# Kernel tuning notes

Hardware: AMD Instinct MI355X
Metric: run time of the kernel (lower is better)

## Reference

```python
import jax, jax.numpy as jnp
import numpy as np

B, NG, DEG, CW, OUT = 8, 16384, 16, 64, 256  # graphs, nodes/graph, avg degree, conv_width, output_dim


def _sage(x, src, dst, mask, Wl, bl, Wr):
    # PyG SAGEConv: mean-aggregate neighbors (src -> dst), lin_l(agg)+bias + lin_r(x)
    N = x.shape[0]
    s = jax.ops.segment_sum(x[src] * mask[:, None], dst, num_segments=N)
    c = jax.ops.segment_sum(mask, dst, num_segments=N)
    mean = s / jnp.maximum(c, 1.0)[:, None]
    return mean @ Wl.T + bl + x @ Wr.T


def _gcn(x, src, dst, mask, W, b):
    # PyG GCNConv: self-loops + symmetric deg^{-1/2} normalization; edge_weight == mask
    N = x.shape[0]
    xw = x @ W.T
    deg = 1.0 + jax.ops.segment_sum(mask, dst, num_segments=N)
    dis = jax.lax.rsqrt(deg)
    norm = dis[src] * mask * dis[dst]
    out = jax.ops.segment_sum(xw[src] * norm[:, None], dst, num_segments=N)
    return out + xw * (dis * dis)[:, None] + b


def _topk(x, src, dst, mask, w, n):
    # PyG TopKPooling: score = tanh(x.w/||w||), keep top ceil(0.5*n) per graph,
    # gate kept features by score, re-index edges (here: fixed-size edges + mask)
    score = jnp.tanh((x @ w) / jnp.linalg.norm(w))
    k = (n + 1) // 2
    vals, idx = jax.lax.top_k(score.reshape(B, n), k)  # [B,k], descending like PyG
    perm = (idx + (jnp.arange(B) * n)[:, None]).reshape(-1)  # global old indices
    x_new = x[perm] * vals.reshape(-1)[:, None]
    newpos = jnp.full((B * n,), -1, jnp.int32).at[perm].set(
        jnp.arange(B * k, dtype=jnp.int32))
    ns, nd = newpos[src], newpos[dst]
    m = mask * ((ns >= 0) & (nd >= 0)).astype(x.dtype)
    return x_new, jnp.maximum(ns, 0), jnp.maximum(nd, 0), m, k


def _readout(x, k):
    # [global_max_pool, global_mean_pool] per graph
    xr = x.reshape(B, k, -1)
    return jnp.concatenate([xr.max(axis=1), xr.mean(axis=1)], axis=1)


def setup_inputs() -> dict:
    key = jax.random.key(0)
    ks = jax.random.split(key, 24)
    N, Eg = B * NG, NG * DEG
    off = (jnp.arange(B) * NG)[:, None]
    src = (jax.random.randint(ks[0], (B, Eg), 0, NG) + off).reshape(-1)
    dst = (jax.random.randint(ks[1], (B, Eg), 0, NG) + off).reshape(-1)
    edge_index = jnp.stack([src, dst]).astype(jnp.int32)
    x = jax.random.normal(ks[2], (N, 2), jnp.float32)

    def xav(k, o, i):
        return jax.random.normal(k, (o, i), jnp.float32) * np.float32(np.sqrt(2.0 / (o + i)))

    def vec(k, d):
        return jax.random.normal(k, (d,), jnp.float32) * np.float32(1.0 / np.sqrt(d))

    return dict(
        x=x, edge_index=edge_index,
        Wl1=xav(ks[3], CW, 2), bl1=vec(ks[4], CW), Wr1=xav(ks[5], CW, 2),
        Wl2=xav(ks[6], CW, CW), bl2=vec(ks[7], CW), Wr2=xav(ks[8], CW, CW),
        W4=xav(ks[9], CW, CW), b4=vec(ks[10], CW),
        W5=xav(ks[11], CW, CW), b5=vec(ks[12], CW),
        wp1=vec(ks[13], CW), wp2=vec(ks[14], CW), wp4=vec(ks[15], CW), wp5=vec(ks[16], CW),
        Wa=xav(ks[17], 128, 2 * CW), ba=vec(ks[18], 128),
        Wb=xav(ks[19], 64, 128), bb=vec(ks[20], 64),
        Wc=xav(ks[21], OUT, 64), bc=vec(ks[22], OUT),
    )


def reference(x, edge_index, Wl1, bl1, Wr1, Wl2, bl2, Wr2, W4, b4, W5, b5,
              wp1, wp2, wp4, wp5, Wa, ba, Wb, bb, Wc, bc):
    src, dst = edge_index[0], edge_index[1]
    mask = jnp.ones(src.shape[0], x.dtype)
    n = NG
    h = jax.nn.relu(_sage(x, src, dst, mask, Wl1, bl1, Wr1))
    h, src, dst, mask, n = _topk(h, src, dst, mask, wp1, n)
    x1 = _readout(h, n)
    h = jax.nn.relu(_sage(h, src, dst, mask, Wl2, bl2, Wr2))
    h, src, dst, mask, n = _topk(h, src, dst, mask, wp2, n)
    x2 = _readout(h, n)
    h = jax.nn.relu(_gcn(h, src, dst, mask, W4, b4))
    h, src, dst, mask, n = _topk(h, src, dst, mask, wp4, n)
    x4 = _readout(h, n)
    h = jax.nn.relu(_gcn(h, src, dst, mask, W5, b5))
    h, src, dst, mask, n = _topk(h, src, dst, mask, wp5, n)
    x5 = _readout(h, n)
    z = x1 + x2 + x4 + x5  # [B, 2*CW]
    z = jax.nn.relu(z @ Wa.T + ba)
    z = jax.nn.relu(z @ Wb.T + bb)
    z = z @ Wc.T + bc
    return jax.nn.softmax(z, axis=1)
```

## Files before the change

kernel.cpp:

```cpp
#include <hip/hip_runtime.h>
#include <math.h>

constexpr int Bq  = 8;
constexpr int NGq = 16384;
constexpr int Nq  = Bq * NGq;
constexpr int Eq  = Nq * 16;
constexpr int Eg  = Eq / 8;
constexpr int BCAP = 8192;

constexpr int P1 = 0;
constexpr int P2 = 524288;
constexpr int P3 = 786432;
constexpr int P4 = 917504;
constexpr int PTOT = 983040;

__global__ void k_prep(const float* __restrict__ Wl2, const float* __restrict__ Wr2,
                       const float* __restrict__ W4, const float* __restrict__ W5,
                       const float* __restrict__ Wa, const float* __restrict__ Wb,
                       const float* __restrict__ Wc,
                       const float* __restrict__ w1, const float* __restrict__ w2,
                       const float* __restrict__ w4p, const float* __restrict__ w5p,
                       float* __restrict__ wT, float* __restrict__ wMT,
                       float* __restrict__ winv, int* __restrict__ bcur) {
    int t = threadIdx.x, b = blockIdx.x;
    if (b < 4) {
        const float* in = (b == 0) ? Wl2 : (b == 1) ? Wr2 : (b == 2) ? W4 : W5;
        float* out = wT + (size_t)b * 4096;
        for (int i = t; i < 4096; i += 256) {
            int r = i >> 6, c = i & 63;
            out[c * 64 + r] = in[r * 64 + c];
        }
    } else if (b == 4) {
        float* WaT = wMT;
        for (int i = t; i < 16384; i += 256) {
            int r = i >> 7, c = i & 127;
            WaT[c * 128 + r] = Wa[r * 128 + c];
        }
    } else if (b == 5) {
        float* WbT = wMT + 16384;
        for (int i = t; i < 8192; i += 256) {
            int r = i >> 7, c = i & 127;
            WbT[c * 64 + r] = Wb[r * 128 + c];
        }
    } else if (b == 6) {
        float* WcT = wMT + 16384 + 8192;
        for (int i = t; i < 16384; i += 256) {
            int r = i >> 6, c = i & 63;
            WcT[c * 256 + r] = Wc[r * 64 + c];
        }
    } else {
        int vsel = t >> 6, lane = t & 63;
        const float* wp = (vsel == 0) ? w1 : (vsel == 1) ? w2 : (vsel == 2) ? w4p : w5p;
        float v = wp[lane];
        float ww = v * v;
        for (int o = 32; o; o >>= 1) ww += __shfl_xor(ww, o);
        if (lane == 0) winv[vsel] = 1.0f / sqrtf(ww);
        for (int i = t; i < 512; i += 256) bcur[i] = 0;
    }
}

__global__ void k_csr_a(const int* __restrict__ src, const int* __restrict__ dst,
                        int* __restrict__ bcur, unsigned* __restrict__ pairs) {
    __shared__ int hist[512];
    __shared__ int base[512];
    __shared__ int lcur[512];
    int t = threadIdx.x;
    int blk = blockIdx.x;
    int e0 = blk * 8192;
    int bk[8]; unsigned p[8];
#pragma unroll
    for (int i = 0; i < 8; i++) {
        int e = e0 + i * 1024 + t;
        int d = dst[e];
        bk[i] = d >> 8;
        p[i] = ((unsigned)(d & 255) << 24) | (unsigned)src[e];
    }
    if (t < 512) hist[t] = 0;
    __syncthreads();
#pragma unroll
    for (int i = 0; i < 8; i++) atomicAdd(&hist[bk[i]], 1);
    __syncthreads();
    if (t < 512) {
        int h = hist[t];
        base[t] = h ? atomicAdd(&bcur[t], h) : 0;
        lcur[t] = 0;
    }
    __syncthreads();
#pragma unroll
    for (int i = 0; i < 8; i++) {
        int b = bk[i];
        int r = base[b] + atomicAdd(&lcur[b], 1);
        if (r < BCAP) pairs[(size_t)b * BCAP + r] = p[i];
    }
}

__global__ void k_csr_b(const int* __restrict__ bcnt, const unsigned* __restrict__ pairs,
                        const float2* __restrict__ x2,
                        int* __restrict__ off, int* __restrict__ deg,
                        int* __restrict__ csrc, float2* __restrict__ mean,
                        const float* __restrict__ Wl1, const float* __restrict__ bl1,
                        const float* __restrict__ Wr1, const float* __restrict__ wp1,
                        const float* __restrict__ invn, float* __restrict__ score) {
    __shared__ int lcnt[256];
    __shared__ int lcur[256];
    __shared__ int wsum[4];
    int b = blockIdx.x, t = threadIdx.x;
    int beg = b * BCAP;
    int c0 = bcnt[b]; if (c0 > BCAP) c0 = BCAP;
    int end = beg + c0;
    lcnt[t] = 0;
    __syncthreads();
    for (int i = beg + t; i < end; i += 256)
        atomicAdd(&lcnt[pairs[i] >> 24], 1);
    __syncthreads();
    int v = lcnt[t];
    int lane = t & 63, wv = t >> 6;
    int val = v;
    for (int o = 1; o < 64; o <<= 1) {
        int u = __shfl_up(val, o);
        if (lane >= o) val += u;
    }
    if (lane == 63) wsum[wv] = val;
    __syncthreads();
    int add = 0;
    for (int q = 0; q < wv; q++) add += wsum[q];
    int gpos = beg + val + add - v;
    off[b * 256 + t] = gpos;
    deg[b * 256 + t] = v;
    lcur[t] = gpos;
    __syncthreads();
    for (int i = beg + t; i < end; i += 256) {
        unsigned p = pairs[i];
        int pos = atomicAdd(&lcur[p >> 24], 1);
        csrc[pos] = (int)(p & 0x00FFFFFFu);
    }
    __syncthreads();
    float s0 = 0.f, s1 = 0.f;
    for (int e = gpos; e < gpos + v; e++) {
        float2 xv = x2[csrc[e]];
        s0 += xv.x; s1 += xv.y;
    }
    float c = fmaxf((float)v, 1.0f);
    float m0 = s0 / c, m1 = s1 / c;
    int n = b * 256 + t;
    mean[n] = make_float2(m0, m1);
    float2 xn = x2[n];
    float dacc = 0.f;
    for (int jj = 0; jj < 64; jj++) {
        float2 wl = ((const float2*)Wl1)[jj];
        float2 wr = ((const float2*)Wr1)[jj];
        float fv = wl.x * m0 + wl.y * m1 + bl1[jj] + wr.x * xn.x + wr.y * xn.y;
        fv = fmaxf(fv, 0.f);
        dacc += fv * wp1[jj];
    }
    score[n] = dacc * invn[0];
}

__device__ __forceinline__
void lin_rows(const float* __restrict__ h, const float* __restrict__ WT,
              const float* __restrict__ bias, float* __restrict__ o,
              int Nn, int nblk, int blk0) {
    int j = threadIdx.x & 63, wv = threadIdx.x >> 6;
    float wreg[64];
#pragma unroll
    for (int q = 0; q < 64; q++) wreg[q] = WT[q * 64 + j];
    float bj = bias ? bias[j] : 0.f;
    int stride = nblk * 4;
    for (int n = blk0 * 4 + wv; n < Nn; n += stride) {
        float iv = h[(size_t)n * 64 + j];
        float a0 = 0.f, a1 = 0.f, a2 = 0.f, a3 = 0.f;
#pragma unroll
        for (int q = 0; q < 16; q++) {
            float s0 = __int_as_float(__builtin_amdgcn_readlane(__float_as_int(iv), q));
            float s1 = __int_as_float(__builtin_amdgcn_readlane(__float_as_int(iv), q + 16));
            float s2 = __int_as_float(__builtin_amdgcn_readlane(__float_as_int(iv), q + 32));
            float s3 = __int_as_float(__builtin_amdgcn_readlane(__float_as_int(iv), q + 48));
            a0 += s0 * wreg[q];
            a1 += s1 * wreg[q + 16];
            a2 += s2 * wreg[q + 32];
            a3 += s3 * wreg[q + 48];
        }
        o[(size_t)n * 64 + j] = (a0 + a1) + (a2 + a3) + bj;
    }
}

__global__ __launch_bounds__(256, 4)
void k_linf(const float* __restrict__ h,
            const float* __restrict__ WT1, float* __restrict__ o1, int linB1,
            const float* __restrict__ WT2, const float* __restrict__ bias,
            float* __restrict__ o2, int linB2,
            int Nn,
            const int* __restrict__ off, const int* __restrict__ deg,
            const int* __restrict__ csrc,
            const int* __restrict__ map, const int* __restrict__ orig,
            float* __restrict__ dis, int ng) {
    int blk = blockIdx.x;
    if (blk < linB1) {
        lin_rows(h, WT1, nullptr, o1, Nn, linB1, blk);
    } else if (blk < linB1 + linB2) {
        lin_rows(h, WT2, bias, o2, Nn, linB2, blk - linB1);
    } else {
        int b2 = blk - linB1 - linB2;
        int g = b2 & 7, i = b2 >> 3;
        int wv = threadIdx.x >> 6, j = threadIdx.x & 63;
        int n = g * ng + i * 4 + wv;
        int o = orig[n];
        int beg = off[o], end = beg + deg[o];
        int c = 0;
        for (int base = beg; base < end; base += 64) {
            int d = end - base; if (d > 64) d = 64;
            int cs = (j < d) ? map[csrc[base + j]] : -1;
            c += __popcll(__ballot(cs >= 0));
        }
        if (j == 0) dis[n] = 1.0f / sqrtf(1.0f + (float)c);
    }
}

template<int M>
__global__ void k_topk(float* __restrict__ score, int* __restrict__ newpos,
                       int* __restrict__ perm, int* __restrict__ map, int mode,
                       const int* __restrict__ orig_in, int* __restrict__ orig_out,
                       int og) {
    constexpr int n = M * 1024;
    constexpr int k = n / 2;
    __shared__ unsigned hist[256];
    __shared__ unsigned sh_pfx, sh_msk, sh_rem;
    __shared__ int sh_eqtot, sh_ctr;
    __shared__ int wtot[16];
    __shared__ int runTie, runGt;
    int t = threadIdx.x, b = blockIdx.x;
    int base = b * n;
    int lane = t & 63, wv = t >> 6;

    unsigned kr[M];
#pragma unroll
    for (int i = 0; i < M; i++) {
        unsigned u = __float_as_uint(score[base + t + (i << 10)]);
        kr[i] = u ^ ((u >> 31) ? 0xFFFFFFFFu : 0x80000000u);
    }
    if (t < 256) hist[t] = 0;
    if (t == 0) { sh_pfx = 0; sh_msk = 0; sh_rem = (unsigned)k;
                  sh_eqtot = 0; sh_ctr = 0; runTie = 0; runGt = 0; }
    __syncthreads();

    for (int shift = 24; shift >= 0; shift -= 8) {
        unsigned pfx = sh_pfx, msk = sh_msk;
#pragma unroll
        for (int i = 0; i < M; i++)
            if ((kr[i] & msk) == pfx) atomicAdd(&hist[(kr[i] >> shift) & 255], 1u);
        __syncthreads();
        if (t < 64) {
            unsigned rem = sh_rem;
            unsigned c0 = hist[255 - (t * 4 + 0)];
            unsigned c1 = hist[255 - (t * 4 + 1)];
            unsigned c2 = hist[255 - (t * 4 + 2)];
            unsigned c3 = hist[255 - (t * 4 + 3)];
            unsigned s = c0 + c1 + c2 + c3;
            unsigned sc = s;
            for (int o = 1; o < 64; o <<= 1) {
                unsigned u = __shfl_up(sc, o);
                if (t >= o) sc += u;
            }
            unsigned run = sc - s;
            unsigned cc[4] = {c0, c1, c2, c3};
#pragma unroll
            for (int q = 0; q < 4; q++) {
                unsigned incl = run + cc[q];
                if (run < rem && incl >= rem) {
                    int bb = 255 - (t * 4 + q);
                    sh_rem = rem - run;
                    sh_pfx = pfx | ((unsigned)bb << shift);
                    sh_msk = msk | (255u << shift);
                }
                run = incl;
            }
        }
        __syncthreads();
        if (t < 256) hist[t] = 0;
        __syncthreads();
    }
    unsigned K = sh_pfx;
    int T = (int)sh_rem;

    int le = 0;
#pragma unroll
    for (int i = 0; i < M; i++) le += (kr[i] == K) ? 1 : 0;
    for (int o = 32; o; o >>= 1) le += __shfl_xor(le, o);
    if (lane == 0) atomicAdd(&sh_eqtot, le);
    __syncthreads();

    if (sh_eqtot == T) {
#pragma unroll
        for (int i = 0; i < M; i++) {
            int cur = base + t + (i << 10);
            bool kept = kr[i] >= K;
            unsigned long long mk = __ballot(kept);
            int pos = 0;
            if (mk) {
                int fl = __ffsll(mk) - 1;
                int bp = 0;
                if (lane == fl) bp = atomicAdd(&sh_ctr, __popcll(mk));
                bp = __shfl(bp, fl);
                pos = bp + __popcll(mk & ((1ull << lane) - 1ull));
            }
            if (kept && pos < k) {
                newpos[cur] = b * k + pos;
                perm[b * k + pos] = cur;
                if (og) orig_out[b * k + pos] = (og == 1) ? cur : orig_in[cur];
                unsigned ob = (kr[i] & 0x80000000u) ? (kr[i] ^ 0x80000000u) : ~kr[i];
                score[cur] = tanhf(__uint_as_float(ob));
            } else newpos[cur] = -1;
        }
    } else {
        for (int i = 0; i < M; i++) {
            unsigned key = kr[i];
            int gt = key > K ? 1 : 0;
            int eq = key == K ? 1 : 0;
            int val = (eq << 16) | gt;
            for (int o = 1; o < 64; o <<= 1) {
                int v = __shfl_up(val, o);
                if (lane >= o) val += v;
            }
            if (lane == 63) wtot[wv] = val;
            __syncthreads();
            int add = 0;
            for (int q = 0; q < 16; q++) if (q < wv) add += wtot[q];
            val += add;
            int eqIncl = val >> 16, gtIncl = val & 0xffff;
            int eqExcl = eqIncl - eq, gtExcl = gtIncl - gt;
            int kept = gt | (eq & ((runTie + eqExcl) < T ? 1 : 0));
            int cur = base + t + (i << 10);
            if (kept) {
                int selEqBefore = runTie + eqExcl; if (selEqBefore > T) selEqBefore = T;
                int nl = runGt + gtExcl + selEqBefore;
                if (nl < k) {
                    newpos[cur] = b * k + nl;
                    perm[b * k + nl] = cur;
                    if (og) orig_out[b * k + nl] = (og == 1) ? cur : orig_in[cur];
                    unsigned ob = (key & 0x80000000u) ? (key ^ 0x80000000u) : ~key;
                    score[cur] = tanhf(__uint_as_float(ob));
                } else newpos[cur] = -1;
            } else newpos[cur] = -1;
            __syncthreads();
            if (t == 1023) { runTie += eqIncl; runGt += gtIncl; }
            __syncthreads();
        }
    }

    if (mode) {
        __syncthreads();
        int gbase = b * NGq;
        for (int i2 = t; i2 < NGq; i2 += 1024) {
            int gi = gbase + i2;
            if (mode == 1) map[gi] = newpos[gi];
            else { int m = map[gi]; map[gi] = (m >= 0) ? newpos[m] : -1; }
        }
    }
}

__global__ void k_compact4(const float* __restrict__ hin, const float* __restrict__ score,
                           const int* __restrict__ perm, float* __restrict__ hout, int k,
                           float* __restrict__ partial) {
    __shared__ float sred[2][16][64];
    int blk = blockIdx.x;
    int g = blk & 7, i = blk >> 3;
    int t = threadIdx.x;
    int r = t >> 4, c = t & 15;
    int nn = g * k + i * 16 + r;
    int old = perm[nn];
    float4 v = ((const float4*)(hin + (size_t)old * 64))[c];
    float sc = score[old];
    v.x *= sc; v.y *= sc; v.z *= sc; v.w *= sc;
    ((float4*)(hout + (size_t)nn * 64))[c] = v;
    sred[0][r][c * 4 + 0] = v.x; sred[0][r][c * 4 + 1] = v.y;
    sred[0][r][c * 4 + 2] = v.z; sred[0][r][c * 4 + 3] = v.w;
    sred[1][r][c * 4 + 0] = v.x; sred[1][r][c * 4 + 1] = v.y;
    sred[1][r][c * 4 + 2] = v.z; sred[1][r][c * 4 + 3] = v.w;
    __syncthreads();
    if (t < 64) {
        float mx = sred[0][0][t], sm = sred[1][0][t];
        for (int rr = 1; rr < 16; rr++) {
            mx = fmaxf(mx, sred[0][rr][t]);
            sm += sred[1][rr][t];
        }
        partial[(size_t)blk * 128 + t] = mx;
        partial[(size_t)blk * 128 + 64 + t] = sm;
    }
}

__global__ void k_compact4r(const float2* __restrict__ mean, const float2* __restrict__ x2,
                            const float* __restrict__ Wl1, const float* __restrict__ bl1,
                            const float* __restrict__ Wr1,
                            const float* __restrict__ score,
                            const int* __restrict__ perm, float* __restrict__ hout, int k,
                            float* __restrict__ partial) {
    __shared__ float sred[2][16][64];
    int blk = blockIdx.x;
    int g = blk & 7, i = blk >> 3;
    int t = threadIdx.x;
    int r = t >> 4, c = t & 15;
    int nn = g * k + i * 16 + r;
    int old = perm[nn];
    float2 m = mean[old];
    float2 xn = x2[old];
    float4 wl01 = ((const float4*)Wl1)[c * 2];
    float4 wl23 = ((const float4*)Wl1)[c * 2 + 1];
    float4 wr01 = ((const float4*)Wr1)[c * 2];
    float4 wr23 = ((const float4*)Wr1)[c * 2 + 1];
    float4 bl   = ((const float4*)bl1)[c];
    float4 v;
    v.x = fmaxf(wl01.x * m.x + wl01.y * m.y + bl.x + wr01.x * xn.x + wr01.y * xn.y, 0.f);
    v.y = fmaxf(wl01.z * m.x + wl01.w * m.y + bl.y + wr01.z * xn.x + wr01.w * xn.y, 0.f);
    v.z = fmaxf(wl23.x * m.x + wl23.y * m.y + bl.z + wr23.x * xn.x + wr23.y * xn.y, 0.f);
    v.w = fmaxf(wl23.z * m.x + wl23.w * m.y + bl.w + wr23.z * xn.x + wr23.w * xn.y, 0.f);
    float sc = score[old];
    v.x *= sc; v.y *= sc; v.z *= sc; v.w *= sc;
    ((float4*)(hout + (size_t)nn * 64))[c] = v;
    sred[0][r][c * 4 + 0] = v.x; sred[0][r][c * 4 + 1] = v.y;
    sred[0][r][c * 4 + 2] = v.z; sred[0][r][c * 4 + 3] = v.w;
    sred[1][r][c * 4 + 0] = v.x; sred[1][r][c * 4 + 1] = v.y;
    sred[1][r][c * 4 + 2] = v.z; sred[1][r][c * 4 + 3] = v.w;
    __syncthreads();
    if (t < 64) {
        float mx = sred[0][0][t], sm = sred[1][0][t];
        for (int rr = 1; rr < 16; rr++) {
            mx = fmaxf(mx, sred[0][rr][t]);
            sm += sred[1][rr][t];
        }
        partial[(size_t)blk * 128 + t] = mx;
        partial[(size_t)blk * 128 + 64 + t] = sm;
    }
}

__global__ void k_sage_gather2(const float* __restrict__ gl, const int* __restrict__ off,
                               const int* __restrict__ deg, const int* __restrict__ csrc,
                               const int* __restrict__ map,
                               const int* __restrict__ orig, const float* __restrict__ wp,
                               const float* __restrict__ invn,
                               float* __restrict__ own_in,
                               float* __restrict__ out, float* __restrict__ score, int ng) {
    int blk = blockIdx.x;
    int g = blk & 7, i = blk >> 3;
    int wv = threadIdx.x >> 6, l = threadIdx.x & 63;
    int n = g * ng + i * 4 + wv;
    int o = orig[n];
    int beg = off[o], end = beg + deg[o];
    int fg = l & 15, es = l >> 4;
    float4 own = make_float4(0.f, 0.f, 0.f, 0.f);
    if (es == 0) own = ((const float4*)(own_in + (size_t)n * 64))[fg];
    float4 acc = make_float4(0.f, 0.f, 0.f, 0.f);
    int cnt = 0;
    for (int base = beg; base < end; base += 64) {
        int d = end - base; if (d > 64) d = 64;
        int cs = (l < d) ? map[csrc[base + l]] : -1;
        cnt += __popcll(__ballot(cs >= 0));
        for (int e = 0; e < d; e += 4) {
            int c = __shfl(cs, e + es);
            if (c >= 0) {
                float4 v = ((const float4*)(gl + (size_t)c * 64))[fg];
                acc.x += v.x; acc.y += v.y; acc.z += v.z; acc.w += v.w;
            }
        }
    }
    acc.x += __shfl_xor(acc.x, 16); acc.y += __shfl_xor(acc.y, 16);
    acc.z += __shfl_xor(acc.z, 16); acc.w += __shfl_xor(acc.w, 16);
    acc.x += __shfl_xor(acc.x, 32); acc.y += __shfl_xor(acc.y, 32);
    acc.z += __shfl_xor(acc.z, 32); acc.w += __shfl_xor(acc.w, 32);
    float c = fmaxf((float)cnt, 1.0f);
    float4 v;
    v.x = fmaxf(acc.x / c + own.x, 0.f);
    v.y = fmaxf(acc.y / c + own.y, 0.f);
    v.z = fmaxf(acc.z / c + own.z, 0.f);
    v.w = fmaxf(acc.w / c + own.w, 0.f);
    float dsc = 0.f;
    if (es == 0) {
        ((float4*)(out + (size_t)n * 64))[fg] = v;
        float4 w4 = ((const float4*)wp)[fg];
        dsc = v.x * w4.x + v.y * w4.y + v.z * w4.z + v.w * w4.w;
    }
    for (int o2 = 32; o2; o2 >>= 1) dsc += __shfl_xor(dsc, o2);
    if (l == 0) score[n] = dsc * invn[0];
}

__global__ void k_gcn_gather(const float* __restrict__ xw, const int* __restrict__ off,
                             const int* __restrict__ deg, const int* __restrict__ csrc,
                             const int* __restrict__ map,
                             const int* __restrict__ orig, const float* __restrict__ dis,
                             const float* __restrict__ bb, const float* __restrict__ wp,
                             const float* __restrict__ invn,
                             float* __restrict__ out, float* __restrict__ score, int ng) {
    int blk = blockIdx.x;
    int g = blk & 7, i = blk >> 3;
    int wv = threadIdx.x >> 6, l = threadIdx.x & 63;
    int n = g * ng + i * 4 + wv;
    int o = orig[n];
    int beg = off[o], end = beg + deg[o];
    int fg = l & 15, es = l >> 4;
    float dn = dis[n];
    float4 own = make_float4(0.f, 0.f, 0.f, 0.f);
    if (es == 0) own = ((const float4*)(xw + (size_t)n * 64))[fg];
    float4 acc = make_float4(0.f, 0.f, 0.f, 0.f);
    for (int base = beg; base < end; base += 64) {
        int d = end - base; if (d > 64) d = 64;
        int cs = -1; float dsv = 0.f;
        if (l < d) {
            int cc = map[csrc[base + l]];
            if (cc >= 0) { cs = cc; dsv = dis[cc]; }
        }
        for (int e = 0; e < d; e += 4) {
            int c = __shfl(cs, e + es);
            float dv = __shfl(dsv, e + es);
            if (c >= 0) {
                float4 v = ((const float4*)(xw + (size_t)c * 64))[fg];
                acc.x += v.x * dv; acc.y += v.y * dv;
                acc.z += v.z * dv; acc.w += v.w * dv;
            }
        }
    }
    acc.x += __shfl_xor(acc.x, 16); acc.y += __shfl_xor(acc.y, 16);
    acc.z += __shfl_xor(acc.z, 16); acc.w += __shfl_xor(acc.w, 16);
    acc.x += __shfl_xor(acc.x, 32); acc.y += __shfl_xor(acc.y, 32);
    acc.z += __shfl_xor(acc.z, 32); acc.w += __shfl_xor(acc.w, 32);
    float dsc = 0.f;
    if (es == 0) {
        float4 b4 = ((const float4*)bb)[fg];
        float dd = dn * dn;
        float4 v;
        v.x = fmaxf(acc.x * dn + own.x * dd + b4.x, 0.f);
        v.y = fmaxf(acc.y * dn + own.y * dd + b4.y, 0.f);
        v.z = fmaxf(acc.z * dn + own.z * dd + b4.z, 0.f);
        v.w = fmaxf(acc.w * dn + own.w * dd + b4.w, 0.f);
        ((float4*)(out + (size_t)n * 64))[fg] = v;
        float4 w4 = ((const float4*)wp)[fg];
        dsc = v.x * w4.x + v.y * w4.y + v.z * w4.z + v.w * w4.w;
    }
    for (int o2 = 32; o2; o2 >>= 1) dsc += __shfl_xor(dsc, o2);
    if (l == 0) score[n] = dsc * invn[0];
}

__global__ void k_zred(const float* __restrict__ part, float* __restrict__ red2) {
    __shared__ float sred[2][128];
    int b2 = blockIdx.x;
    int g = b2 & 7, slice = b2 >> 3;
    int t = threadIdx.x;
    int j = t & 127, h = t >> 7;
    int pb0 = slice * 60 + h * 30;
    float accm = -3.0e38f, accs = 0.f;
    for (int pb = pb0; pb < pb0 + 30; pb++) {
        const float* p; int i; float scale;
        if (pb < 512)      { p = part + P1; i = pb;       scale = 1.0f / 8192.0f; }
        else if (pb < 768) { p = part + P2; i = pb - 512; scale = 1.0f / 4096.0f; }
        else if (pb < 896) { p = part + P3; i = pb - 768; scale = 1.0f / 2048.0f; }
        else               { p = part + P4; i = pb - 896; scale = 1.0f / 1024.0f; }
        float v = p[(size_t)(i * 8 + g) * 128 + j];
        accm = fmaxf(accm, v);
        accs += v * scale;
    }
    sred[h][j] = (j < 64) ? accm : accs;
    __syncthreads();
    if (t < 128) {
        float out = (j < 64) ? fmaxf(sred[0][j], sred[1][j]) : (sred[0][j] + sred[1][j]);
        red2[(size_t)b2 * 128 + j] = out;
    }
}

__global__ void k_mlpz(const float* __restrict__ red2,
                       const float* __restrict__ WaT, const float* __restrict__ ba,
                       const float* __restrict__ WbT, const float* __restrict__ bb,
                       const float* __restrict__ WcT, const float* __restrict__ bc,
                       float* __restrict__ out) {
    __shared__ float red[8][128];
    __shared__ float sz[128];
    __shared__ float sa[128];
    __shared__ float sb2[64];
    __shared__ float sc[256];
    __shared__ float tmp[256];
    __shared__ float wred[4];
    int b = blockIdx.x, t = threadIdx.x;
    int j = t & 127, s = t >> 7;
    {
        float v0 = red2[(size_t)((s * 2 + 0) * 8 + b) * 128 + j];
        float v1 = red2[(size_t)((s * 2 + 1) * 8 + b) * 128 + j];
        red[s][j] = (j < 64) ? fmaxf(v0, v1) : (v0 + v1);
    }
    __syncthreads();
    if (t < 128) {
        float zv;
        if (j < 64) {
            float m1 = fmaxf(fmaxf(red[0][j], red[1][j]), fmaxf(red[2][j], red[3][j]));
            float m2 = fmaxf(fmaxf(red[4][j], red[5][j]), fmaxf(red[6][j], red[7][j]));
            zv = fmaxf(m1, m2);
        } else {
            zv = ((red[0][j] + red[1][j]) + (red[2][j] + red[3][j]))
               + ((red[4][j] + red[5][j]) + (red[6][j] + red[7][j]));
        }
        sz[t] = zv;
    }
    __syncthreads();
    if (t < 256) {
        int o = t & 127, half = t >> 7;
        float v = 0.f;
        int q0 = half * 64;
        for (int q = q0; q < q0 + 64; q++) v += sz[q] * WaT[q * 128 + o];
        tmp[t] = v;
    }
    __syncthreads();
    if (t < 128) sa[t] = fmaxf(tmp[t] + tmp[t + 128] + ba[t], 0.f);
    __syncthreads();
    if (t < 256) {
        int o = t & 63, qr = t >> 6;
        float v = 0.f;
        int q0 = qr * 32;
        for (int q = q0; q < q0 + 32; q++) v += sa[q] * WbT[q * 64 + o];
        tmp[t] = v;
    }
    __syncthreads();
    if (t < 64) sb2[t] = fmaxf(tmp[t] + tmp[t + 64] + tmp[t + 128] + tmp[t + 192] + bb[t], 0.f);
    __syncthreads();
    if (t < 256) {
        float v = bc[t];
        for (int q = 0; q < 64; q++) v += sb2[q] * WcT[q * 256 + t];
        sc[t] = v;
    }
    __syncthreads();
    if (t < 256) {
        float m = sc[t];
        for (int o2 = 32; o2; o2 >>= 1) m = fmaxf(m, __shfl_xor(m, o2));
        if ((t & 63) == 0) wred[t >> 6] = m;
    }
    __syncthreads();
    float m = fmaxf(fmaxf(wred[0], wred[1]), fmaxf(wred[2], wred[3]));
    __syncthreads();
    if (t < 256) {
        float e = expf(sc[t] - m);
        tmp[t] = e;
        float ss = e;
        for (int o2 = 32; o2; o2 >>= 1) ss += __shfl_xor(ss, o2);
        if ((t & 63) == 0) wred[t >> 6] = ss;
    }
    __syncthreads();
    if (t < 256) {
        float ss = wred[0] + wred[1] + wred[2] + wred[3];
        out[b * 256 + t] = tmp[t] / ss;
    }
}

extern "C" void kernel_launch(void* const* d_in, const int* in_sizes, int n_in,
                              void* d_out, int out_size, void* d_ws, size_t ws_size,
                              hipStream_t stream) {
    const float* x   = (const float*)d_in[0];
    const int*   ei  = (const int*)d_in[1];
    const int* src = ei;
    const int* dst = ei + Eq;
    const float* Wl1 = (const float*)d_in[2];
    const float* bl1 = (const float*)d_in[3];
    const float* Wr1 = (const float*)d_in[4];
    const float* Wl2 = (const float*)d_in[5];
    const float* bl2 = (const float*)d_in[6];
    const float* Wr2 = (const float*)d_in[7];
    const float* W4  = (const float*)d_in[8];
    const float* b4  = (const float*)d_in[9];
    const float* W5  = (const float*)d_in[10];
    const float* b5  = (const float*)d_in[11];
    const float* wp1 = (const float*)d_in[12];
    const float* wp2 = (const float*)d_in[13];
    const float* wp4 = (const float*)d_in[14];
    const float* wp5 = (const float*)d_in[15];
    const float* Wa  = (const float*)d_in[16];
    const float* ba  = (const float*)d_in[17];
    const float* Wb  = (const float*)d_in[18];
    const float* bbv = (const float*)d_in[19];
    const float* Wc  = (const float*)d_in[20];
    const float* bc  = (const float*)d_in[21];
    float* out = (float*)d_out;

    const int N1 = Nq / 2, N2 = Nq / 4, N3 = Nq / 8, N4 = Nq / 16;

    char* w = (char*)d_ws;
    float* hA    = (float*)w; w += (size_t)Nq * 64 * 4;
    float* hB    = (float*)w; w += (size_t)N1 * 64 * 4;
    float* hC    = (float*)w; w += (size_t)N1 * 64 * 4;
    int*   csrc  = (int*)w;   w += (size_t)512 * BCAP * 4;
    int*   coff  = (int*)w;   w += (size_t)(Nq + 1) * 4;
    int*   degA  = (int*)w;   w += (size_t)Nq * 4;
    int*   bcur  = (int*)w;   w += (size_t)Nq * 4;
    int*   cnt   = (int*)w;   w += (size_t)Nq * 4;
    float* dis   = (float*)w; w += (size_t)Nq * 4;
    float* score = (float*)w; w += (size_t)Nq * 4;
    int*   newpos= (int*)w;   w += (size_t)Nq * 4;
    int*   map   = (int*)w;   w += (size_t)Nq * 4;
    int*   perm  = (int*)w;   w += (size_t)Nq * 4;
    int*   origA = (int*)w;   w += (size_t)Nq * 4;
    int*   origB = (int*)w;   w += (size_t)Nq * 4;
    float* part  = (float*)w; w += (size_t)PTOT * 4;
    float* red2  = (float*)w; w += (size_t)128 * 128 * 4;
    float* wT    = (float*)w; w += 4 * 4096 * 4;
    float* wMT   = (float*)w; w += (16384 + 8192 + 16384) * 4;
    float* WlT2 = wT, *WrT2 = wT + 4096, *W4T = wT + 8192, *W5T = wT + 12288;
    float* WaT = wMT, *WbT = wMT + 16384, *WcT = wMT + 16384 + 8192;
    unsigned* pairs = (unsigned*)hA;
    float2* mean = (float2*)cnt;
    float* winv = (float*)(bcur + 1024);

    k_prep<<<8, 256, 0, stream>>>(Wl2, Wr2, W4, W5, Wa, Wb, Wc,
                                  wp1, wp2, wp4, wp5, wT, wMT, winv, bcur);
    k_csr_a<<<256, 1024, 0, stream>>>(src, dst, bcur, pairs);
    k_csr_b<<<512, 256, 0, stream>>>(bcur, pairs, (const float2*)x, coff, degA, csrc, mean,
                                     Wl1, bl1, Wr1, wp1, winv, score);

    k_topk<16><<<8, 1024, 0, stream>>>(score, newpos, perm, map, 1, nullptr, origA, 1);
    k_compact4r<<<N1 / 16, 256, 0, stream>>>(mean, (const float2*)x, Wl1, bl1, Wr1,
                                             score, perm, hB, N1 / 8, part + P1);

    k_linf<<<512 + 512, 256, 0, stream>>>(hB,
                                          WlT2, hC, 512,
                                          WrT2, bl2, hA, 512,
                                          N1,
                                          nullptr, nullptr, nullptr, nullptr, nullptr,
                                          nullptr, 0);
    k_sage_gather2<<<N1 / 4, 256, 0, stream>>>(hC, coff, degA, csrc, map, origA,
                                               wp2, winv + 1, hA, hA, score, N1 / 8);
    k_topk<8><<<8, 1024, 0, stream>>>(score, newpos, perm, map, 2, origA, origB, 2);
    k_compact4<<<N2 / 16, 256, 0, stream>>>(hA, score, perm, hB, N2 / 8, part + P2);

    k_linf<<<512 + 8192, 256, 0, stream>>>(hB,
                                           W4T, hC, 512,
                                           nullptr, nullptr, nullptr, 0,
                                           N2,
                                           coff, degA, csrc, map, origB,
                                           dis, N2 / 8);
    k_gcn_gather<<<N2 / 4, 256, 0, stream>>>(hC, coff, degA, csrc, map, origB, dis,
                                             b4, wp4, winv + 2, hA, score, N2 / 8);
    k_topk<4><<<8, 1024, 0, stream>>>(score, newpos, perm, map, 2, origB, origA, 2);
    k_compact4<<<N3 / 16, 256, 0, stream>>>(hA, score, perm, hB, N3 / 8, part + P3);

    k_linf<<<256 + 4096, 256, 0, stream>>>(hB,
                                           W5T, hC, 256,
                                           nullptr, nullptr, nullptr, 0,
                                           N3,
                                           coff, degA, csrc, map, origA,
                                           dis, N3 / 8);
    k_gcn_gather<<<N3 / 4, 256, 0, stream>>>(hC, coff, degA, csrc, map, origA, dis,
                                             b5, wp5, winv + 3, hA, score, N3 / 8);
    k_topk<2><<<8, 1024, 0, stream>>>(score, newpos, perm, map, 0, nullptr, nullptr, 0);
    k_compact4<<<N4 / 16, 256, 0, stream>>>(hA, score, perm, hB, N4 / 8, part + P4);

    k_zred<<<128, 256, 0, stream>>>(part, red2);
    k_mlpz<<<8, 1024, 0, stream>>>(red2, WaT, ba, WbT, bbv, WcT, bc, out);
}
```

Before: 417.6 us.

## Split per-graph top-k into grid-wide histogram, select, and compaction kernels

Replaces the single-block-per-graph radix-select top-k (8 blocks of 1024 threads) with three kernels: a grid-wide 16-bit-prefix histogram built with global atomics, a per-graph selection kernel that scans the 65536-bin histogram and refines the low 16 bits, and a grid-wide compaction that assigns output positions with global atomic counters. The map update that used to run at the end of top-k now runs in extra blocks appended to the compact kernels. The goal is to spread top-k across the whole GPU instead of 8 CUs, at the cost of a large histogram memset, more launches, and output order that depends on atomic scheduling rather than a fixed order.

```diff
diff --git a/kernel.cpp b/kernel.cpp
--- a/kernel.cpp
+++ b/kernel.cpp
@@ -216,155 +216,155 @@
     }
 }
 
-template<int M>
-__global__ void k_topk(float* __restrict__ score, int* __restrict__ newpos,
-                       int* __restrict__ perm, int* __restrict__ map, int mode,
-                       const int* __restrict__ orig_in, int* __restrict__ orig_out,
-                       int og) {
-    constexpr int n = M * 1024;
-    constexpr int k = n / 2;
-    __shared__ unsigned hist[256];
-    __shared__ unsigned sh_pfx, sh_msk, sh_rem;
-    __shared__ int sh_eqtot, sh_ctr;
-    __shared__ int wtot[16];
-    __shared__ int runTie, runGt;
-    int t = threadIdx.x, b = blockIdx.x;
-    int base = b * n;
+__global__ void k_thist(const float* __restrict__ score, int* __restrict__ hist,
+                        int lg2n) {
+    int t = threadIdx.x;
+#pragma unroll
+    for (int i = 0; i < 4; i++) {
+        int idx = blockIdx.x * 1024 + i * 256 + t;
+        unsigned u = __float_as_uint(score[idx]);
+        unsigned key = u ^ ((u >> 31) ? 0xFFFFFFFFu : 0x80000000u);
+        atomicAdd(&hist[((idx >> lg2n) << 16) + (key >> 16)], 1);
+    }
+}
+
+__global__ void k_tsel(const int* __restrict__ hist, const float* __restrict__ score,
+                       int n, int k, unsigned* __restrict__ Kv,
+                       int* __restrict__ tie, int* __restrict__ pctr) {
+    __shared__ int chunk[16];
+    __shared__ int sh_bin, sh_rem;
+    __shared__ int lhist[256];
+    __shared__ unsigned sh_pfx16;
+    __shared__ int sh_rem2;
+    int g = blockIdx.x, t = threadIdx.x;
     int lane = t & 63, wv = t >> 6;
-
-    unsigned kr[M];
-#pragma unroll
-    for (int i = 0; i < M; i++) {
-        unsigned u = __float_as_uint(score[base + t + (i << 10)]);
-        kr[i] = u ^ ((u >> 31) ? 0xFFFFFFFFu : 0x80000000u);
-    }
-    if (t < 256) hist[t] = 0;
-    if (t == 0) { sh_pfx = 0; sh_msk = 0; sh_rem = (unsigned)k;
-                  sh_eqtot = 0; sh_ctr = 0; runTie = 0; runGt = 0; }
-    __syncthreads();
-
-    for (int shift = 24; shift >= 0; shift -= 8) {
-        unsigned pfx = sh_pfx, msk = sh_msk;
-#pragma unroll
-        for (int i = 0; i < M; i++)
-            if ((kr[i] & msk) == pfx) atomicAdd(&hist[(kr[i] >> shift) & 255], 1u);
+    const int* h = hist + (g << 16);
+    if (t == 0) { sh_bin = 0; sh_rem = k; }
+    int base = 65536 - 64 * (t + 1);
+    int s = 0;
+    for (int i = 0; i < 64; i++) s += h[base + i];
+    int val = s;
+    for (int o = 1; o < 64; o <<= 1) {
+        int u = __shfl_up(val, o);
+        if (lane >= o) val += u;
+    }
+    if (lane == 63) chunk[wv] = val;
+    __syncthreads();
+    int add = 0;
+    for (int q = 0; q < wv; q++) add += chunk[q];
+    int incl = val + add;
+    int excl = incl - s;
+    if (excl < k && incl >= k) {
+        int run = excl;
+        for (int i = 63; i >= 0; i--) {
+            int c = h[base + i];
+            if (c > 0 && run + c >= k) { sh_bin = base + i; sh_rem = k - run; break; }
+            run += c;
+        }
+    }
+    __syncthreads();
+    unsigned B = (unsigned)sh_bin;
+    int rem = sh_rem;
+    if (t == 0) { sh_pfx16 = 0; sh_rem2 = rem; }
+    __syncthreads();
+    unsigned msk16 = 0;
+    for (int shift = 8; shift >= 0; shift -= 8) {
+        unsigned pfx16 = sh_pfx16;
+        if (t < 256) lhist[t] = 0;
+        __syncthreads();
+        for (int e = t; e < n; e += 1024) {
+            unsigned u = __float_as_uint(score[(size_t)g * n + e]);
+            unsigned key = u ^ ((u >> 31) ? 0xFFFFFFFFu : 0x80000000u);
+            if ((key >> 16) == B && ((key & 0xFFFFu) & msk16) == pfx16)
+                atomicAdd(&lhist[(key >> shift) & 255], 1);
+        }
         __syncthreads();
         if (t < 64) {
-            unsigned rem = sh_rem;
-            unsigned c0 = hist[255 - (t * 4 + 0)];
-            unsigned c1 = hist[255 - (t * 4 + 1)];
-            unsigned c2 = hist[255 - (t * 4 + 2)];
-            unsigned c3 = hist[255 - (t * 4 + 3)];
-            unsigned s = c0 + c1 + c2 + c3;
-            unsigned sc = s;
+            unsigned remu = (unsigned)sh_rem2;
+            unsigned c0 = lhist[255 - (t * 4 + 0)];
+            unsigned c1 = lhist[255 - (t * 4 + 1)];
+            unsigned c2 = lhist[255 - (t * 4 + 2)];
+            unsigned c3 = lhist[255 - (t * 4 + 3)];
+            unsigned s2 = c0 + c1 + c2 + c3;
+            unsigned sc2 = s2;
             for (int o = 1; o < 64; o <<= 1) {
-                unsigned u = __shfl_up(sc, o);
-                if (t >= o) sc += u;
+                unsigned uu = __shfl_up(sc2, o);
+                if (t >= o) sc2 += uu;
             }
-            unsigned run = sc - s;
+            unsigned run = sc2 - s2;
             unsigned cc[4] = {c0, c1, c2, c3};
 #pragma unroll
             for (int q = 0; q < 4; q++) {
-                unsigned incl = run + cc[q];
-                if (run < rem && incl >= rem) {
+                unsigned incl2 = run + cc[q];
+                if (run < remu && incl2 >= remu) {
                     int bb = 255 - (t * 4 + q);
-                    sh_rem = rem - run;
-                    sh_pfx = pfx | ((unsigned)bb << shift);
-                    sh_msk = msk | (255u << shift);
+                    sh_rem2 = (int)(remu - run);
+                    sh_pfx16 = pfx16 | ((unsigned)bb << shift);
                 }
-                run = incl;
+                run = incl2;
             }
         }
         __syncthreads();
-        if (t < 256) hist[t] = 0;
-        __syncthreads();
-    }
-    unsigned K = sh_pfx;
-    int T = (int)sh_rem;
-
-    int le = 0;
+        msk16 |= (255u << shift);
+    }
+    if (t == 0) {
+        Kv[g] = (B << 16) | sh_pfx16;
+        int tt = sh_rem2; if (tt < 0) tt = 0; if (tt > k) tt = k;
+        tie[g] = tt;
+        pctr[g] = 0;
+    }
+}
+
+__global__ void k_tkcomp(float* __restrict__ score, const unsigned* __restrict__ Kv,
+                         int* __restrict__ tie, int* __restrict__ pctr,
+                         int* __restrict__ newpos, int* __restrict__ perm,
+                         const int* __restrict__ orig_in, int* __restrict__ orig_out,
+                         int og, int k, int lg2n) {
+    int t = threadIdx.x;
+    int g = (blockIdx.x * 1024) >> lg2n;
+    unsigned K = Kv[g];
+    int lane = t & 63;
 #pragma unroll
-    for (int i = 0; i < M; i++) le += (kr[i] == K) ? 1 : 0;
-    for (int o = 32; o; o >>= 1) le += __shfl_xor(le, o);
-    if (lane == 0) atomicAdd(&sh_eqtot, le);
-    __syncthreads();
-
-    if (sh_eqtot == T) {
-#pragma unroll
-        for (int i = 0; i < M; i++) {
-            int cur = base + t + (i << 10);
-            bool kept = kr[i] >= K;
-            unsigned long long mk = __ballot(kept);
-            int pos = 0;
-            if (mk) {
-                int fl = __ffsll(mk) - 1;
-                int bp = 0;
-                if (lane == fl) bp = atomicAdd(&sh_ctr, __popcll(mk));
-                bp = __shfl(bp, fl);
-                pos = bp + __popcll(mk & ((1ull << lane) - 1ull));
-            }
-            if (kept && pos < k) {
-                newpos[cur] = b * k + pos;
-                perm[b * k + pos] = cur;
-                if (og) orig_out[b * k + pos] = (og == 1) ? cur : orig_in[cur];
-                unsigned ob = (kr[i] & 0x80000000u) ? (kr[i] ^ 0x80000000u) : ~kr[i];
-                score[cur] = tanhf(__uint_as_float(ob));
-            } else newpos[cur] = -1;
-        }
-    } else {
-        for (int i = 0; i < M; i++) {
-            unsigned key = kr[i];
-            int gt = key > K ? 1 : 0;
-            int eq = key == K ? 1 : 0;
-            int val = (eq << 16) | gt;
-            for (int o = 1; o < 64; o <<= 1) {
-                int v = __shfl_up(val, o);
-                if (lane >= o) val += v;
-            }
-            if (lane == 63) wtot[wv] = val;
-            __syncthreads();
-            int add = 0;
-            for (int q = 0; q < 16; q++) if (q < wv) add += wtot[q];
-            val += add;
-            int eqIncl = val >> 16, gtIncl = val & 0xffff;
-            int eqExcl = eqIncl - eq, gtExcl = gtIncl - gt;
-            int kept = gt | (eq & ((runTie + eqExcl) < T ? 1 : 0));
-            int cur = base + t + (i << 10);
-            if (kept) {
-                int selEqBefore = runTie + eqExcl; if (selEqBefore > T) selEqBefore = T;
-                int nl = runGt + gtExcl + selEqBefore;
-                if (nl < k) {
-                    newpos[cur] = b * k + nl;
-                    perm[b * k + nl] = cur;
-                    if (og) orig_out[b * k + nl] = (og == 1) ? cur : orig_in[cur];
-                    unsigned ob = (key & 0x80000000u) ? (key ^ 0x80000000u) : ~key;
-                    score[cur] = tanhf(__uint_as_float(ob));
-                } else newpos[cur] = -1;
-            } else newpos[cur] = -1;
-            __syncthreads();
-            if (t == 1023) { runTie += eqIncl; runGt += gtIncl; }
-            __syncthreads();
-        }
-    }
-
-    if (mode) {
-        __syncthreads();
-        int gbase = b * NGq;
-        for (int i2 = t; i2 < NGq; i2 += 1024) {
-            int gi = gbase + i2;
-            if (mode == 1) map[gi] = newpos[gi];
-            else { int m = map[gi]; map[gi] = (m >= 0) ? newpos[m] : -1; }
-        }
+    for (int i = 0; i < 4; i++) {
+        int e = blockIdx.x * 1024 + i * 256 + t;
+        float sv = score[e];
+        unsigned u = __float_as_uint(sv);
+        unsigned key = u ^ ((u >> 31) ? 0xFFFFFFFFu : 0x80000000u);
+        bool kept = key > K;
+        if (key == K) kept = (atomicSub(&tie[g], 1) > 0);
+        unsigned long long mk = __ballot(kept);
+        int pos = -1;
+        if (mk) {
+            int fl = __ffsll(mk) - 1;
+            int bp = 0;
+            if (lane == fl) bp = atomicAdd(&pctr[g], __popcll(mk));
+            bp = __shfl(bp, fl);
+            pos = bp + __popcll(mk & ((1ull << lane) - 1ull));
+        }
+        if (kept && pos >= 0 && pos < k) {
+            newpos[e] = g * k + pos;
+            perm[g * k + pos] = e;
+            if (og) orig_out[g * k + pos] = (og == 1) ? e : orig_in[e];
+            score[e] = tanhf(sv);
+        } else newpos[e] = -1;
     }
 }
 
 __global__ void k_compact4(const float* __restrict__ hin, const float* __restrict__ score,
                            const int* __restrict__ perm, float* __restrict__ hout, int k,
-                           float* __restrict__ partial) {
+                           float* __restrict__ partial,
+                           const int* __restrict__ newpos, int* __restrict__ map,
+                           int mode, int mainB) {
     __shared__ float sred[2][16][64];
     int blk = blockIdx.x;
+    int t = threadIdx.x;
+    if (blk >= mainB) {
+        int gi = (blk - mainB) * 256 + t;
+        if (mode == 1) map[gi] = newpos[gi];
+        else { int m = map[gi]; map[gi] = (m >= 0) ? newpos[m] : -1; }
+        return;
+    }
     int g = blk & 7, i = blk >> 3;
-    int t = threadIdx.x;
     int r = t >> 4, c = t & 15;
     int nn = g * k + i * 16 + r;
     int old = perm[nn];
@@ -393,11 +393,19 @@
                             const float* __restrict__ Wr1,
                             const float* __restrict__ score,
                             const int* __restrict__ perm, float* __restrict__ hout, int k,
-                            float* __restrict__ partial) {
+                            float* __restrict__ partial,
+                            const int* __restrict__ newpos, int* __restrict__ map,
+                            int mode, int mainB) {
     __shared__ float sred[2][16][64];
     int blk = blockIdx.x;
+    int t = threadIdx.x;
+    if (blk >= mainB) {
+        int gi = (blk - mainB) * 256 + t;
+        if (mode == 1) map[gi] = newpos[gi];
+        else { int m = map[gi]; map[gi] = (m >= 0) ? newpos[m] : -1; }
+        return;
+    }
     int g = blk & 7, i = blk >> 3;
-    int t = threadIdx.x;
     int r = t >> 4, c = t & 15;
     int nn = g * k + i * 16 + r;
     int old = perm[nn];
@@ -694,6 +702,7 @@
     int*   origB = (int*)w;   w += (size_t)Nq * 4;
     float* part  = (float*)w; w += (size_t)PTOT * 4;
     float* red2  = (float*)w; w += (size_t)128 * 128 * 4;
+    int*   thist = (int*)w;   w += (size_t)4 * 8 * 65536 * 4;
     float* wT    = (float*)w; w += 4 * 4096 * 4;
     float* wMT   = (float*)w; w += (16384 + 8192 + 16384) * 4;
     float* WlT2 = wT, *WrT2 = wT + 4096, *W4T = wT + 8192, *W5T = wT + 12288;
@@ -701,16 +710,24 @@
     unsigned* pairs = (unsigned*)hA;
     float2* mean = (float2*)cnt;
     float* winv = (float*)(bcur + 1024);
+    unsigned* Kv = (unsigned*)(bcur + 2048);
+    int* tieq   = bcur + 2064;
+    int* pctr   = bcur + 2080;
 
     k_prep<<<8, 256, 0, stream>>>(Wl2, Wr2, W4, W5, Wa, Wb, Wc,
                                   wp1, wp2, wp4, wp5, wT, wMT, winv, bcur);
+    hipMemsetAsync(thist, 0, (size_t)4 * 8 * 65536 * 4, stream);
     k_csr_a<<<256, 1024, 0, stream>>>(src, dst, bcur, pairs);
     k_csr_b<<<512, 256, 0, stream>>>(bcur, pairs, (const float2*)x, coff, degA, csrc, mean,
                                      Wl1, bl1, Wr1, wp1, winv, score);
 
-    k_topk<16><<<8, 1024, 0, stream>>>(score, newpos, perm, map, 1, nullptr, origA, 1);
-    k_compact4r<<<N1 / 16, 256, 0, stream>>>(mean, (const float2*)x, Wl1, bl1, Wr1,
-                                             score, perm, hB, N1 / 8, part + P1);
+    k_thist<<<Nq / 1024, 256, 0, stream>>>(score, thist, 14);
+    k_tsel<<<8, 1024, 0, stream>>>(thist, score, NGq, NGq / 2, Kv, tieq, pctr);
+    k_tkcomp<<<Nq / 1024, 256, 0, stream>>>(score, Kv, tieq, pctr, newpos, perm,
+                                            nullptr, origA, 1, NGq / 2, 14);
+    k_compact4r<<<4096 + 512, 256, 0, stream>>>(mean, (const float2*)x, Wl1, bl1, Wr1,
+                                                score, perm, hB, N1 / 8, part + P1,
+                                                newpos, map, 1, 4096);
 
     k_linf<<<512 + 512, 256, 0, stream>>>(hB,
                                           WlT2, hC, 512,
@@ -720,8 +737,12 @@
                                           nullptr, 0);
     k_sage_gather2<<<N1 / 4, 256, 0, stream>>>(hC, coff, degA, csrc, map, origA,
                                                wp2, winv + 1, hA, hA, score, N1 / 8);
-    k_topk<8><<<8, 1024, 0, stream>>>(score, newpos, perm, map, 2, origA, origB, 2);
-    k_compact4<<<N2 / 16, 256, 0, stream>>>(hA, score, perm, hB, N2 / 8, part + P2);
+    k_thist<<<N1 / 1024, 256, 0, stream>>>(score, thist + 524288, 13);
+    k_tsel<<<8, 1024, 0, stream>>>(thist + 524288, score, NGq / 2, NGq / 4, Kv, tieq, pctr);
+    k_tkcomp<<<N1 / 1024, 256, 0, stream>>>(score, Kv, tieq, pctr, newpos, perm,
+                                            origA, origB, 2, NGq / 4, 13);
+    k_compact4<<<2048 + 512, 256, 0, stream>>>(hA, score, perm, hB, N2 / 8, part + P2,
+                                               newpos, map, 2, 2048);
 
     k_linf<<<512 + 8192, 256, 0, stream>>>(hB,
                                            W4T, hC, 512,
@@ -731,8 +752,12 @@
                                            dis, N2 / 8);
     k_gcn_gather<<<N2 / 4, 256, 0, stream>>>(hC, coff, degA, csrc, map, origB, dis,
                                              b4, wp4, winv + 2, hA, score, N2 / 8);
-    k_topk<4><<<8, 1024, 0, stream>>>(score, newpos, perm, map, 2, origB, origA, 2);
-    k_compact4<<<N3 / 16, 256, 0, stream>>>(hA, score, perm, hB, N3 / 8, part + P3);
+    k_thist<<<N2 / 1024, 256, 0, stream>>>(score, thist + 2 * 524288, 12);
+    k_tsel<<<8, 1024, 0, stream>>>(thist + 2 * 524288, score, NGq / 4, NGq / 8, Kv, tieq, pctr);
+    k_tkcomp<<<N2 / 1024, 256, 0, stream>>>(score, Kv, tieq, pctr, newpos, perm,
+                                            origB, origA, 2, NGq / 8, 12);
+    k_compact4<<<1024 + 512, 256, 0, stream>>>(hA, score, perm, hB, N3 / 8, part + P3,
+                                               newpos, map, 2, 1024);
 
     k_linf<<<256 + 4096, 256, 0, stream>>>(hB,
                                            W5T, hC, 256,
@@ -742,8 +767,12 @@
                                            dis, N3 / 8);
     k_gcn_gather<<<N3 / 4, 256, 0, stream>>>(hC, coff, degA, csrc, map, origA, dis,
                                              b5, wp5, winv + 3, hA, score, N3 / 8);
-    k_topk<2><<<8, 1024, 0, stream>>>(score, newpos, perm, map, 0, nullptr, nullptr, 0);
-    k_compact4<<<N4 / 16, 256, 0, stream>>>(hA, score, perm, hB, N4 / 8, part + P4);
+    k_thist<<<N3 / 1024, 256, 0, stream>>>(score, thist + 3 * 524288, 11);
+    k_tsel<<<8, 1024, 0, stream>>>(thist + 3 * 524288, score, NGq / 8, NGq / 16, Kv, tieq, pctr);
+    k_tkcomp<<<N3 / 1024, 256, 0, stream>>>(score, Kv, tieq, pctr, newpos, perm,
+                                            nullptr, nullptr, 0, NGq / 16, 11);
+    k_compact4<<<512, 256, 0, stream>>>(hA, score, perm, hB, N4 / 8, part + P4,
+                                        newpos, map, 0, 512);
 
     k_zred<<<128, 256, 0, stream>>>(part, red2);
     k_mlpz<<<8, 1024, 0, stream>>>(red2, WaT, ba, WbT, bbv, WcT, bc, out);
```

After: 505.2 us. 1.21x slower.
